# Kernel optimization log

Measured on AMD Instinct MI355X. Metric: run time of the kernel, lower is better.

Reference implementation:

```python
import jax, jax.numpy as jnp
import numpy as np

N, E, F, H = 50000, 800000, 128, 128
HEADS, HOUT, NUM_GRAPHS, NUM_CLASSES, L = 4, 32, 50, 2, 3
BN_EPS = 1e-5


def setup_inputs() -> dict:
    key = jax.random.key(0)
    it = iter(jax.random.split(key, 64))
    def nrm(shape, scale=0.1):
        return scale * jax.random.normal(next(it), shape, jnp.float32)
    npg = N // NUM_GRAPHS  # nodes per graph = 1000
    # edges constrained to stay within a single graph
    src = jax.random.randint(next(it), (E,), 0, npg, jnp.int32)
    dst = jax.random.randint(next(it), (E,), 0, npg, jnp.int32)
    goff = jax.random.randint(next(it), (E,), 0, NUM_GRAPHS, jnp.int32) * npg
    return dict(
        x=jax.random.normal(next(it), (N, F), jnp.float32),
        edge_index=jnp.stack([src + goff, dst + goff]),
        batch=jnp.arange(N, dtype=jnp.int32) // npg,
        W_gcn=nrm((F, H)), b_gcn=nrm((H,)),
        gin_W1=nrm((F, H)), gin_b1=nrm((H,)), gin_W2=nrm((H, H)), gin_b2=nrm((H,)),
        W_gat=nrm((F, HEADS * HOUT)), b_gat=nrm((HEADS * HOUT,)),
        a_src=nrm((HEADS, HOUT)), a_dst=nrm((HEADS, HOUT)),
        gat_proj_W=nrm((HEADS * HOUT, H)), gat_proj_b=nrm((H,)),
        gate_W1=nrm((3 * H, H)), gate_b1=nrm((H,)), gate_W2=nrm((H, 3)), gate_b2=nrm((3,)),
        bn0_g=jnp.ones((H,), jnp.float32) + nrm((H,)), bn0_b=nrm((H,)),
        conv_rel_W=nrm((L, H, H)), conv_rel_b=nrm((L, H)), conv_root_W=nrm((L, H, H)),
        bn_g=jnp.ones((L, H), jnp.float32) + nrm((L, H)), bn_b=nrm((L, H)),
        jump_W=nrm((L * H, H)), jump_b=nrm((H,)),
        att_W1=nrm((H, H)), att_b1=nrm((H,)), att_W2=nrm((H, 1)), att_b2=nrm((1,)),
        comb_W=nrm((4 * H, H)), comb_b=nrm((H,)),
        cls_W1=nrm((H, H // 2)), cls_b1=nrm((H // 2,)),
        cls_W2=nrm((H // 2, NUM_CLASSES)), cls_b2=nrm((NUM_CLASSES,)),
    )


def _forward(x, edge_index, batch, W_gcn, b_gcn, gin_W1, gin_b1, gin_W2, gin_b2,
             W_gat, b_gat, a_src, a_dst, gat_proj_W, gat_proj_b,
             gate_W1, gate_b1, gate_W2, gate_b2, bn0_g, bn0_b,
             conv_rel_W, conv_rel_b, conv_root_W, bn_g, bn_b, jump_W, jump_b,
             att_W1, att_b1, att_W2, att_b2, comb_W, comb_b,
             cls_W1, cls_b1, cls_W2, cls_b2):
    relu = jax.nn.relu
    seg_sum, seg_max = jax.ops.segment_sum, jax.ops.segment_max
    n = x.shape[0]
    src, dst = edge_index[0], edge_index[1]
    loop = jnp.arange(n, dtype=src.dtype)
    src_sl = jnp.concatenate([src, loop])  # self-loops (GCN/GAT add them)
    dst_sl = jnp.concatenate([dst, loop])

    def bn(h, g, b):  # eval-mode BatchNorm1d, running mean=0, var=1
        return h * (g / jnp.sqrt(1.0 + BN_EPS)) + b

    # --- GCN stem: sym-normalized A+I ---
    deg = seg_sum(jnp.ones_like(dst_sl, jnp.float32), dst_sl, num_segments=n)
    dinv = jax.lax.rsqrt(deg)  # deg >= 1 thanks to self-loops
    norm = dinv[src_sl] * dinv[dst_sl]
    h = x @ W_gcn
    x_gcn = relu(seg_sum(h[src_sl] * norm[:, None], dst_sl, num_segments=n) + b_gcn)

    # --- GIN stem: MLP((1+0)*x + sum_j x_j), no self-loops ---
    aggr = seg_sum(x[src], dst, num_segments=n)
    x_gin = relu(relu((x + aggr) @ gin_W1 + gin_b1) @ gin_W2 + gin_b2)

    # --- GAT stem: per-edge attention, segment softmax over dst ---
    xp = (x @ W_gat).reshape(n, HEADS, HOUT)
    al_s = (xp * a_src).sum(-1)  # [n, heads]
    al_d = (xp * a_dst).sum(-1)
    e = jax.nn.leaky_relu(al_s[src_sl] + al_d[dst_sl], 0.2)  # [E+n, heads]
    m = seg_max(e, dst_sl, num_segments=n)
    ex = jnp.exp(e - m[dst_sl])
    alpha = ex / seg_sum(ex, dst_sl, num_segments=n)[dst_sl]
    x_gat = seg_sum(xp[src_sl] * alpha[:, :, None], dst_sl, num_segments=n)
    x_gat = x_gat.reshape(n, HEADS * HOUT) + b_gat
    x_gat = relu(x_gat) @ gat_proj_W + gat_proj_b

    # --- gated fusion ---
    x_cat = jnp.concatenate([x_gcn, x_gin, x_gat], axis=-1)
    gates = jax.nn.softmax(relu(x_cat @ gate_W1 + gate_b1) @ gate_W2 + gate_b2, axis=-1)
    xx = gates[:, 0:1] * x_gcn + gates[:, 1:2] * x_gin + gates[:, 2:3] * x_gat
    xx = relu(bn(xx, bn0_g, bn0_b))  # dropout = no-op in eval

    # --- GraphConv stack with residuals (IdentityPooling since use_sag=False) ---
    reps = []
    for i in range(L):
        x_in = xx
        a = seg_sum(xx[src], dst, num_segments=n)  # aggr='add'
        h = a @ conv_rel_W[i] + conv_rel_b[i] + xx @ conv_root_W[i]
        xx = relu(bn(h, bn_g[i], bn_b[i])) + x_in
        reps.append(xx)

    xx = jnp.concatenate(reps, axis=-1) @ jump_W + jump_b  # JK cat

    # --- combo global pooling: mean / max / add / att ---
    cnt = seg_sum(jnp.ones((n,), jnp.float32), batch, num_segments=NUM_GRAPHS)
    x_add = seg_sum(xx, batch, num_segments=NUM_GRAPHS)
    x_mean = x_add / cnt[:, None]
    x_max = seg_max(xx, batch, num_segments=NUM_GRAPHS)
    a_log = (relu(xx @ att_W1 + att_b1) @ att_W2 + att_b2)[:, 0]  # [n]
    mg = seg_max(a_log, batch, num_segments=NUM_GRAPHS)
    exg = jnp.exp(a_log - mg[batch])
    att = exg / seg_sum(exg, batch, num_segments=NUM_GRAPHS)[batch]
    x_att = seg_sum(xx * att[:, None], batch, num_segments=NUM_GRAPHS)
    hg = jnp.concatenate([x_mean, x_max, x_add, x_att], axis=-1) @ comb_W + comb_b

    return relu(hg @ cls_W1 + cls_b1) @ cls_W2 + cls_b2  # [NUM_GRAPHS, NUM_CLASSES]


def reference(x, edge_index, batch, W_gcn, b_gcn, gin_W1, gin_b1, gin_W2, gin_b2,
              W_gat, b_gat, a_src, a_dst, gat_proj_W, gat_proj_b,
              gate_W1, gate_b1, gate_W2, gate_b2, bn0_g, bn0_b,
              conv_rel_W, conv_rel_b, conv_root_W, bn_g, bn_b, jump_W, jump_b,
              att_W1, att_b1, att_W2, att_b2, comb_W, comb_b,
              cls_W1, cls_b1, cls_W2, cls_b2):
    return _forward(x, edge_index, batch, W_gcn, b_gcn, gin_W1, gin_b1, gin_W2, gin_b2,
                    W_gat, b_gat, a_src, a_dst, gat_proj_W, gat_proj_b,
                    gate_W1, gate_b1, gate_W2, gate_b2, bn0_g, bn0_b,
                    conv_rel_W, conv_rel_b, conv_root_W, bn_g, bn_b, jump_W, jump_b,
                    att_W1, att_b1, att_W2, att_b2, comb_W, comb_b,
                    cls_W1, cls_b1, cls_W2, cls_b2)
```

## Files before the change

### kernel.cpp

```cpp
#include <hip/hip_runtime.h>

typedef float f32x4 __attribute__((ext_vector_type(4)));
typedef short s16x8 __attribute__((ext_vector_type(8)));

#define LDA 136

static __device__ __forceinline__ unsigned short f2bf(float f){
  union { float f; unsigned int u; } v; v.f = f;
  unsigned int u = v.u;
  return (unsigned short)((u + 0x7fffu + ((u >> 16) & 1u)) >> 16);
}
static __device__ __forceinline__ float2 bfp2f(unsigned int p){
  union { unsigned int u; float f; } a, b;
  a.u = (p & 0xffffu) << 16; b.u = p & 0xffff0000u;
  return make_float2(a.f, b.f);
}
static __device__ __forceinline__ unsigned int f2bfp(float x, float y){
  return (unsigned int)f2bf(x) | ((unsigned int)f2bf(y) << 16);
}
static __device__ __forceinline__ float bf2f(unsigned short h){
  union { unsigned int u; float f; } v; v.u = (unsigned int)h << 16; return v.f;
}

static __device__ __forceinline__ float lrelu02(float x){ return x > 0.f ? x : 0.2f * x; }

static __device__ __forceinline__ int xcd_swz(int bid, int nwg){
  int q = nwg >> 3, r = nwg & 7, x = bid & 7, i = bid >> 3;
  return (x < r ? x * (q + 1) : r * (q + 1) + (x - r) * q) + i;
}


__global__ void zero_u32(unsigned int* p, int n){
  int i = blockIdx.x * 256 + threadIdx.x;
  if (i < n) p[i] = 0u;
}

__global__ void gcount_kernel(const int* __restrict__ dst, unsigned int* __restrict__ gcnt,
                              int E, int npg, int ng){
  __shared__ unsigned int h[64];
  int tid = threadIdx.x;
  if (tid < 64) h[tid] = 0u;
  __syncthreads();
  for (int i = blockIdx.x * 256 + tid; i < E; i += gridDim.x * 256)
    atomicAdd(&h[dst[i] / npg], 1u);
  __syncthreads();
  if (tid < ng) atomicAdd(&gcnt[tid], h[tid]);
}

__global__ void gscan_kernel(const unsigned int* __restrict__ gcnt, unsigned int* __restrict__ goff, int ng){
  if (threadIdx.x == 0){
    unsigned int run = 0;
    for (int i = 0; i < ng; ++i){ goff[i] = run; run += gcnt[i]; }
    goff[ng] = run;
  }
}

__global__ void gbucket_kernel(const int* __restrict__ src, const int* __restrict__ dst,
                               const unsigned int* __restrict__ goff, unsigned int* __restrict__ gfill,
                               int2* __restrict__ ebuf, int E, int npg, int ng){
  __shared__ unsigned int h[64];
  __shared__ unsigned int base[64];
  __shared__ unsigned int fl[64];
  int tid = threadIdx.x;
  if (tid < 64){ h[tid] = 0u; fl[tid] = 0u; }
  __syncthreads();
  int per = (E + gridDim.x - 1) / gridDim.x;
  int i0 = blockIdx.x * per, i1 = min(E, i0 + per);
  for (int i = i0 + tid; i < i1; i += 256)
    atomicAdd(&h[dst[i] / npg], 1u);
  __syncthreads();
  if (tid < ng) base[tid] = goff[tid] + atomicAdd(&gfill[tid], h[tid]);
  __syncthreads();
  for (int i = i0 + tid; i < i1; i += 256){
    int d = dst[i];
    int g = d / npg;
    unsigned int p = base[g] + atomicAdd(&fl[g], 1u);
    ebuf[p] = make_int2(src[i], d);
  }
}

__global__ void csr_graph_kernel(const int2* __restrict__ ebuf, const unsigned int* __restrict__ goff,
                                 unsigned int* __restrict__ rp, int* __restrict__ colA,
                                 int* __restrict__ dstA, float* __restrict__ dinv,
                                 int npg, int N, int Etot){
  __shared__ unsigned int hist[1024];
  __shared__ unsigned int fill[1024];
  int g = blockIdx.x, tid = threadIdx.x;
  unsigned int e0 = goff[g], e1 = goff[g + 1];
  int nbase = g * npg;
  hist[tid] = 0u; fill[tid] = 0u;
  __syncthreads();
  for (unsigned int e = e0 + tid; e < e1; e += 1024)
    atomicAdd(&hist[ebuf[e].y - nbase], 1u);
  __syncthreads();
  unsigned int cnt = hist[tid];
  for (int off = 1; off < 1024; off <<= 1){
    unsigned int t = (tid >= off) ? hist[tid - off] : 0u;
    __syncthreads();
    hist[tid] += t;
    __syncthreads();
  }
  unsigned int basev = e0 + hist[tid] - cnt;
  __syncthreads();
  hist[tid] = basev;
  if (tid < npg){
    int node = nbase + tid;
    rp[node] = basev;
    dinv[node] = rsqrtf((float)cnt + 1.0f);
  }
  if (g == 0 && tid == 0) rp[N] = (unsigned int)Etot;
  __syncthreads();
  for (unsigned int e = e0 + tid; e < e1; e += 1024){
    int2 sd = ebuf[e];
    int ld = sd.y - nbase;
    unsigned int pos = hist[ld] + atomicAdd(&fill[ld], 1u);
    colA[pos] = sd.x;
    dstA[pos] = sd.y;
  }
}

__global__ void xcast_kernel(const float* __restrict__ x, unsigned short* __restrict__ xb, int n2){
  int i = blockIdx.x * 256 + threadIdx.x;
  if (i < n2){
    float2 v = ((const float2*)x)[i];
    ((unsigned int*)xb)[i] = f2bfp(v.x, v.y);
  }
}

__global__ void ew_kernel(const int* __restrict__ colA, const int* __restrict__ dstA,
                          const float* __restrict__ als, const float* __restrict__ ald,
                          unsigned int* __restrict__ wb, int E){
  int i = blockIdx.x * 256 + threadIdx.x;
  if (i >= E) return;
  int s = colA[i], d = dstA[i];
  float4 as = ((const float4*)als)[s];
  float4 ad = ((const float4*)ald)[d];
  float w0 = __expf(fminf(lrelu02(as.x + ad.x), 30.f));
  float w1 = __expf(fminf(lrelu02(as.y + ad.y), 30.f));
  float w2 = __expf(fminf(lrelu02(as.z + ad.z), 30.f));
  float w3 = __expf(fminf(lrelu02(as.w + ad.w), 30.f));
  wb[(size_t)i * 2 + 0] = f2bfp(w0, w1);
  wb[(size_t)i * 2 + 1] = f2bfp(w2, w3);
}


struct WSrc { const float* p[18]; };

__global__ void wtrans_kernel(WSrc s, unsigned short* __restrict__ dstAll){
  const float* src = s.p[blockIdx.x];
  unsigned short* dst = dstAll + (size_t)blockIdx.x * 16384;
  __shared__ float st[64][129];
  int tid = threadIdx.x;
  int kb = blockIdx.y * 64;
#pragma unroll
  for (int j = 0; j < 8; ++j){
    int e = tid + 256 * j;
    int r = e >> 5, c4 = (e & 31) * 4;
    float4 v = *(const float4*)(src + (size_t)(kb + r) * 128 + c4);
    st[r][c4] = v.x; st[r][c4+1] = v.y; st[r][c4+2] = v.z; st[r][c4+3] = v.w;
  }
  __syncthreads();
#pragma unroll
  for (int j = 0; j < 8; ++j){
    int e = tid + 256 * j;
    int c = e >> 4, k4 = (e & 15) * 4;
    ushort4 o;
    o.x = f2bf(st[k4+0][c]); o.y = f2bf(st[k4+1][c]);
    o.z = f2bf(st[k4+2][c]); o.w = f2bf(st[k4+3][c]);
    *(ushort4*)(dst + (size_t)c * 128 + kb + k4) = o;
  }
}


template<int EPI>
__launch_bounds__(256, 2)
__global__ void gemm_kernel(const unsigned short* __restrict__ A0, const unsigned short* __restrict__ A1,
                            const unsigned short* __restrict__ A2,
                            const unsigned short* __restrict__ W0, const unsigned short* __restrict__ W1,
                            const unsigned short* __restrict__ W2,
                            const float* __restrict__ bias, const float* __restrict__ bng, const float* __restrict__ bnb,
                            const unsigned short* __restrict__ resid, unsigned short* __restrict__ C, int nrows)
{
  __shared__ unsigned short As[64 * LDA];
  __shared__ unsigned short Wt[128 * LDA];
  const int tid = threadIdx.x;
  const int wave = tid >> 6, lane = tid & 63;
  const int row0 = blockIdx.x * 64;
  const unsigned short* Aps[3] = {A0, A1, A2};
  const unsigned short* Wps[3] = {W0, W1, W2};
  f32x4 acc[8];
#pragma unroll
  for (int i = 0; i < 8; ++i) acc[i] = (f32x4){0.f, 0.f, 0.f, 0.f};

  for (int p = 0; p < 3; ++p){
    const unsigned short* Ap = Aps[p];
    if (Ap == nullptr) break;
    const unsigned short* Wp = Wps[p];
    if (p) __syncthreads();
#pragma unroll
    for (int j = 0; j < 4; ++j){
      int e = tid + 256 * j;
      int r = e >> 4, k8 = (e & 15) * 8;
      int gr = row0 + r;
      s16x8 v = {0,0,0,0,0,0,0,0};
      if (gr < nrows) v = *(const s16x8*)(Ap + (size_t)gr * 128 + k8);
      *(s16x8*)(As + r * LDA + k8) = v;
    }
#pragma unroll
    for (int j = 0; j < 8; ++j){
      int e = tid + 256 * j;
      int colw = e >> 4, k8 = (e & 15) * 8;
      *(s16x8*)(Wt + colw * LDA + k8) = *(const s16x8*)(Wp + (size_t)colw * 128 + k8);
    }
    __syncthreads();
#pragma unroll
    for (int kc = 0; kc < 4; ++kc){
      int ko = kc * 32 + (lane >> 4) * 8;
      s16x8 av = *(const s16x8*)(As + (wave * 16 + (lane & 15)) * LDA + ko);
#pragma unroll
      for (int ct = 0; ct < 8; ++ct){
        s16x8 bv = *(const s16x8*)(Wt + (ct * 16 + (lane & 15)) * LDA + ko);
        acc[ct] = __builtin_amdgcn_mfma_f32_16x16x32_bf16(av, bv, acc[ct], 0, 0, 0);
      }
    }
  }
  const float RSQ = 0.99999500003749969f;
#pragma unroll
  for (int ct = 0; ct < 8; ++ct){
    int colg = ct * 16 + (lane & 15);
    float bv_ = (EPI >= 1) ? bias[colg] : 0.f;
    float sg = (EPI == 3) ? bng[colg] * RSQ : 0.f;
    float sb = (EPI == 3) ? bnb[colg] : 0.f;
#pragma unroll
    for (int r = 0; r < 4; ++r){
      int rowg = row0 + wave * 16 + (lane >> 4) * 4 + r;
      if (rowg < nrows){
        float v = acc[ct][r];
        if (EPI == 1) v += bv_;
        else if (EPI == 2) v = fmaxf(v + bv_, 0.f);
        else if (EPI == 3){
          v = (v + bv_) * sg + sb;
          v = fmaxf(v, 0.f) + bf2f(resid[(size_t)rowg * 128 + colg]);
        }
        C[(size_t)rowg * 128 + colg] = f2bf(v);
      }
    }
  }
}

__launch_bounds__(256, 2)
__global__ void gemm_dual_kernel(const unsigned short* __restrict__ A,
                                 const unsigned short* __restrict__ W0, const unsigned short* __restrict__ W1,
                                 const float* __restrict__ dscale,
                                 unsigned short* __restrict__ C0, unsigned short* __restrict__ C1, int nrows)
{
  __shared__ unsigned short As[64 * LDA];
  __shared__ unsigned short Wt[128 * LDA];
  const int tid = threadIdx.x;
  const int wave = tid >> 6, lane = tid & 63;
  const int row0 = blockIdx.x * 64;
  f32x4 acc0[8], acc1[8];
#pragma unroll
  for (int i = 0; i < 8; ++i){ acc0[i] = (f32x4){0.f,0.f,0.f,0.f}; acc1[i] = (f32x4){0.f,0.f,0.f,0.f}; }

#pragma unroll
  for (int j = 0; j < 4; ++j){
    int e = tid + 256 * j;
    int r = e >> 4, k8 = (e & 15) * 8;
    int gr = row0 + r;
    s16x8 v = {0,0,0,0,0,0,0,0};
    if (gr < nrows) v = *(const s16x8*)(A + (size_t)gr * 128 + k8);
    *(s16x8*)(As + r * LDA + k8) = v;
  }
#pragma unroll
  for (int j = 0; j < 8; ++j){
    int e = tid + 256 * j;
    int colw = e >> 4, k8 = (e & 15) * 8;
    *(s16x8*)(Wt + colw * LDA + k8) = *(const s16x8*)(W0 + (size_t)colw * 128 + k8);
  }
  __syncthreads();
  s16x8 av[4];
#pragma unroll
  for (int kc = 0; kc < 4; ++kc)
    av[kc] = *(const s16x8*)(As + (wave * 16 + (lane & 15)) * LDA + kc * 32 + (lane >> 4) * 8);
#pragma unroll
  for (int kc = 0; kc < 4; ++kc){
    int ko = kc * 32 + (lane >> 4) * 8;
#pragma unroll
    for (int ct = 0; ct < 8; ++ct){
      s16x8 bv = *(const s16x8*)(Wt + (ct * 16 + (lane & 15)) * LDA + ko);
      acc0[ct] = __builtin_amdgcn_mfma_f32_16x16x32_bf16(av[kc], bv, acc0[ct], 0, 0, 0);
    }
  }
  __syncthreads();
#pragma unroll
  for (int j = 0; j < 8; ++j){
    int e = tid + 256 * j;
    int colw = e >> 4, k8 = (e & 15) * 8;
    *(s16x8*)(Wt + colw * LDA + k8) = *(const s16x8*)(W1 + (size_t)colw * 128 + k8);
  }
  __syncthreads();
#pragma unroll
  for (int kc = 0; kc < 4; ++kc){
    int ko = kc * 32 + (lane >> 4) * 8;
#pragma unroll
    for (int ct = 0; ct < 8; ++ct){
      s16x8 bv = *(const s16x8*)(Wt + (ct * 16 + (lane & 15)) * LDA + ko);
      acc1[ct] = __builtin_amdgcn_mfma_f32_16x16x32_bf16(av[kc], bv, acc1[ct], 0, 0, 0);
    }
  }
#pragma unroll
  for (int ct = 0; ct < 8; ++ct){
    int colg = ct * 16 + (lane & 15);
#pragma unroll
    for (int r = 0; r < 4; ++r){
      int rowg = row0 + wave * 16 + (lane >> 4) * 4 + r;
      if (rowg < nrows){
        C0[(size_t)rowg * 128 + colg] = f2bf(acc0[ct][r] * dscale[rowg]);
        C1[(size_t)rowg * 128 + colg] = f2bf(acc1[ct][r]);
      }
    }
  }
}


__global__ void gin_agg_kernel(const unsigned short* __restrict__ x, const unsigned int* __restrict__ rp,
                               const int* __restrict__ col, unsigned short* __restrict__ xs, int n){
  int bid = xcd_swz(blockIdx.x, gridDim.x);
  int node = bid * 4 + (int)(threadIdx.x >> 6);
  if (node >= n) return;
  int lane = threadIdx.x & 63;
  const unsigned int* xin = (const unsigned int*)x;
  float2 acc = bfp2f(xin[(size_t)node * 64 + lane]);
  unsigned int rs = rp[node], re = rp[node + 1], e = rs;
  for (; e + 4 <= re; e += 4){
    int s0 = col[e], s1 = col[e+1], s2 = col[e+2], s3 = col[e+3];
    float2 v0 = bfp2f(xin[(size_t)s0 * 64 + lane]);
    float2 v1 = bfp2f(xin[(size_t)s1 * 64 + lane]);
    float2 v2 = bfp2f(xin[(size_t)s2 * 64 + lane]);
    float2 v3 = bfp2f(xin[(size_t)s3 * 64 + lane]);
    acc.x += v0.x + v1.x + v2.x + v3.x;
    acc.y += v0.y + v1.y + v2.y + v3.y;
  }
  for (; e < re; ++e){
    float2 v = bfp2f(xin[(size_t)col[e] * 64 + lane]);
    acc.x += v.x; acc.y += v.y;
  }
  ((unsigned int*)xs)[(size_t)node * 64 + lane] = f2bfp(acc.x, acc.y);
}

__global__ void gcn_agg_kernel(const unsigned short* __restrict__ hd, const float* __restrict__ dinv,
                               const unsigned int* __restrict__ rp, const int* __restrict__ col,
                               const float* __restrict__ b, unsigned short* __restrict__ out, int n){
  int bid = xcd_swz(blockIdx.x, gridDim.x);
  int node = bid * 4 + (int)(threadIdx.x >> 6);
  if (node >= n) return;
  int lane = threadIdx.x & 63;
  const unsigned int* hv = (const unsigned int*)hd;
  float di = dinv[node];
  float2 acc = bfp2f(hv[(size_t)node * 64 + lane]);
  unsigned int rs = rp[node], re = rp[node + 1], e = rs;
  for (; e + 4 <= re; e += 4){
    int s0 = col[e], s1 = col[e+1], s2 = col[e+2], s3 = col[e+3];
    float2 v0 = bfp2f(hv[(size_t)s0 * 64 + lane]);
    float2 v1 = bfp2f(hv[(size_t)s1 * 64 + lane]);
    float2 v2 = bfp2f(hv[(size_t)s2 * 64 + lane]);
    float2 v3 = bfp2f(hv[(size_t)s3 * 64 + lane]);
    acc.x += v0.x + v1.x + v2.x + v3.x;
    acc.y += v0.y + v1.y + v2.y + v3.y;
  }
  for (; e < re; ++e){
    float2 v = bfp2f(hv[(size_t)col[e] * 64 + lane]);
    acc.x += v.x; acc.y += v.y;
  }
  int f = lane * 2;
  float o0 = fmaxf(acc.x * di + b[f], 0.f);
  float o1 = fmaxf(acc.y * di + b[f + 1], 0.f);
  ((unsigned int*)out)[(size_t)node * 64 + lane] = f2bfp(o0, o1);
}

__global__ void sum_agg_kernel(const unsigned short* __restrict__ x, const unsigned int* __restrict__ rp,
                               const int* __restrict__ col, unsigned short* __restrict__ out, int n){
  int bid = xcd_swz(blockIdx.x, gridDim.x);
  int node = bid * 4 + (int)(threadIdx.x >> 6);
  if (node >= n) return;
  int lane = threadIdx.x & 63;
  const unsigned int* xin = (const unsigned int*)x;
  float2 acc = make_float2(0.f, 0.f);
  unsigned int rs = rp[node], re = rp[node + 1], e = rs;
  for (; e + 4 <= re; e += 4){
    int s0 = col[e], s1 = col[e+1], s2 = col[e+2], s3 = col[e+3];
    float2 v0 = bfp2f(xin[(size_t)s0 * 64 + lane]);
    float2 v1 = bfp2f(xin[(size_t)s1 * 64 + lane]);
    float2 v2 = bfp2f(xin[(size_t)s2 * 64 + lane]);
    float2 v3 = bfp2f(xin[(size_t)s3 * 64 + lane]);
    acc.x += v0.x + v1.x + v2.x + v3.x;
    acc.y += v0.y + v1.y + v2.y + v3.y;
  }
  for (; e < re; ++e){
    float2 v = bfp2f(xin[(size_t)col[e] * 64 + lane]);
    acc.x += v.x; acc.y += v.y;
  }
  ((unsigned int*)out)[(size_t)node * 64 + lane] = f2bfp(acc.x, acc.y);
}

__global__ void gat_agg_kernel(const unsigned short* __restrict__ xp, const float* __restrict__ als,
                               const float* __restrict__ ald, const unsigned int* __restrict__ wb,
                               const unsigned int* __restrict__ rp, const int* __restrict__ col,
                               const float* __restrict__ bgat, unsigned short* __restrict__ out, int n){
  int bid = xcd_swz(blockIdx.x, gridDim.x);
  int node = bid * 4 + (int)(threadIdx.x >> 6);
  if (node >= n) return;
  int lane = threadIdx.x & 63;
  int h = lane >> 4;
  int wword = h >> 1, wsh = (h & 1) * 16;
  const unsigned int* xv = (const unsigned int*)xp;
  float w = __expf(fminf(lrelu02(als[(size_t)node * 4 + h] + ald[(size_t)node * 4 + h]), 30.f));
  float2 sv = bfp2f(xv[(size_t)node * 64 + lane]);
  float2 acc = make_float2(sv.x * w, sv.y * w);
  float denom = w;
  unsigned int rs = rp[node], re = rp[node + 1], e = rs;
  for (; e + 4 <= re; e += 4){
    int s0 = col[e], s1 = col[e+1], s2 = col[e+2], s3 = col[e+3];
    float w0 = bf2f((unsigned short)(wb[(size_t)(e+0) * 2 + wword] >> wsh));
    float w1 = bf2f((unsigned short)(wb[(size_t)(e+1) * 2 + wword] >> wsh));
    float w2 = bf2f((unsigned short)(wb[(size_t)(e+2) * 2 + wword] >> wsh));
    float w3 = bf2f((unsigned short)(wb[(size_t)(e+3) * 2 + wword] >> wsh));
    float2 v0 = bfp2f(xv[(size_t)s0 * 64 + lane]);
    float2 v1 = bfp2f(xv[(size_t)s1 * 64 + lane]);
    float2 v2 = bfp2f(xv[(size_t)s2 * 64 + lane]);
    float2 v3 = bfp2f(xv[(size_t)s3 * 64 + lane]);
    acc.x += v0.x * w0 + v1.x * w1 + v2.x * w2 + v3.x * w3;
    acc.y += v0.y * w0 + v1.y * w1 + v2.y * w2 + v3.y * w3;
    denom += w0 + w1 + w2 + w3;
  }
  for (; e < re; ++e){
    float we = bf2f((unsigned short)(wb[(size_t)e * 2 + wword] >> wsh));
    float2 v = bfp2f(xv[(size_t)col[e] * 64 + lane]);
    acc.x += v.x * we; acc.y += v.y * we;
    denom += we;
  }
  float inv = 1.0f / denom;
  int f = lane * 2;
  float o0 = fmaxf(acc.x * inv + bgat[f], 0.f);
  float o1 = fmaxf(acc.y * inv + bgat[f + 1], 0.f);
  ((unsigned int*)out)[(size_t)node * 64 + lane] = f2bfp(o0, o1);
}


__global__ void alpair_kernel(const unsigned short* __restrict__ xp, const float* __restrict__ a_src,
                              const float* __restrict__ a_dst, float* __restrict__ als,
                              float* __restrict__ ald, int n){
  int node = blockIdx.x * 4 + (int)(threadIdx.x >> 6);
  if (node >= n) return;
  int lane = threadIdx.x & 63;
  int f = lane * 2;
  float2 v = bfp2f(((const unsigned int*)xp)[(size_t)node * 64 + lane]);
  float ps = v.x * a_src[f] + v.y * a_src[f + 1];
  float pd = v.x * a_dst[f] + v.y * a_dst[f + 1];
#pragma unroll
  for (int off = 1; off < 16; off <<= 1){
    ps += __shfl_xor(ps, off, 64);
    pd += __shfl_xor(pd, off, 64);
  }
  if ((lane & 15) == 0){
    int hh = lane >> 4;
    als[(size_t)node * 4 + hh] = ps;
    ald[(size_t)node * 4 + hh] = pd;
  }
}

__global__ void combine_kernel(const unsigned short* __restrict__ t, const float* __restrict__ W2,
                               const float* __restrict__ b2, const unsigned short* __restrict__ xg,
                               const unsigned short* __restrict__ xi, const unsigned short* __restrict__ xa,
                               const float* __restrict__ bn0g, const float* __restrict__ bn0b,
                               unsigned short* __restrict__ xx, int n){
  int node = blockIdx.x * 4 + (int)(threadIdx.x >> 6);
  if (node >= n) return;
  int lane = threadIdx.x & 63;
  int f = lane * 2;
  float2 tv = bfp2f(((const unsigned int*)t)[(size_t)node * 64 + lane]);
  float p0 = tv.x * W2[f * 3 + 0] + tv.y * W2[(f + 1) * 3 + 0];
  float p1 = tv.x * W2[f * 3 + 1] + tv.y * W2[(f + 1) * 3 + 1];
  float p2 = tv.x * W2[f * 3 + 2] + tv.y * W2[(f + 1) * 3 + 2];
#pragma unroll
  for (int off = 1; off < 64; off <<= 1){
    p0 += __shfl_xor(p0, off, 64);
    p1 += __shfl_xor(p1, off, 64);
    p2 += __shfl_xor(p2, off, 64);
  }
  p0 += b2[0]; p1 += b2[1]; p2 += b2[2];
  float mm = fmaxf(p0, fmaxf(p1, p2));
  float e0 = __expf(p0 - mm), e1 = __expf(p1 - mm), e2 = __expf(p2 - mm);
  float inv = 1.0f / (e0 + e1 + e2);
  e0 *= inv; e1 *= inv; e2 *= inv;
  float2 a = bfp2f(((const unsigned int*)xg)[(size_t)node * 64 + lane]);
  float2 b = bfp2f(((const unsigned int*)xi)[(size_t)node * 64 + lane]);
  float2 c = bfp2f(((const unsigned int*)xa)[(size_t)node * 64 + lane]);
  const float RSQ = 0.99999500003749969f;
  float o0 = fmaxf((e0 * a.x + e1 * b.x + e2 * c.x) * (bn0g[f] * RSQ) + bn0b[f], 0.f);
  float o1 = fmaxf((e0 * a.y + e1 * b.y + e2 * c.y) * (bn0g[f + 1] * RSQ) + bn0b[f + 1], 0.f);
  ((unsigned int*)xx)[(size_t)node * 64 + lane] = f2bfp(o0, o1);
}

__global__ void alog_kernel(const unsigned short* __restrict__ t, const float* __restrict__ w,
                            const float* __restrict__ b, float* __restrict__ alog, int n){
  int node = blockIdx.x * 4 + (int)(threadIdx.x >> 6);
  if (node >= n) return;
  int lane = threadIdx.x & 63;
  int f = lane * 2;
  float2 tv = bfp2f(((const unsigned int*)t)[(size_t)node * 64 + lane]);
  float p = tv.x * w[f] + tv.y * w[f + 1];
#pragma unroll
  for (int off = 1; off < 64; off <<= 1) p += __shfl_xor(p, off, 64);
  if (lane == 0) alog[node] = p + b[0];
}


__global__ void att_stats_kernel(const float* __restrict__ alog, float* __restrict__ gm,
                                 float* __restrict__ gz, int npg){
  __shared__ float red[256];
  int g = blockIdx.x, tid = threadIdx.x;
  size_t base = (size_t)g * npg;
  float m = -1e30f;
  for (int i = tid; i < npg; i += 256) m = fmaxf(m, alog[base + i]);
  red[tid] = m; __syncthreads();
  for (int off = 128; off > 0; off >>= 1){ if (tid < off) red[tid] = fmaxf(red[tid], red[tid + off]); __syncthreads(); }
  float gmax = red[0]; __syncthreads();
  float z = 0.f;
  for (int i = tid; i < npg; i += 256) z += __expf(alog[base + i] - gmax);
  red[tid] = z; __syncthreads();
  for (int off = 128; off > 0; off >>= 1){ if (tid < off) red[tid] += red[tid + off]; __syncthreads(); }
  if (tid == 0){ gm[g] = gmax; gz[g] = red[0]; }
}

__global__ void pool_partial_kernel(const unsigned short* __restrict__ xx, const float* __restrict__ alog,
                                    const float* __restrict__ gm, const float* __restrict__ gz,
                                    float* __restrict__ part, int npg, int nparts){
  __shared__ float wts[128];
  __shared__ float red[256];
  int g = blockIdx.x / nparts, p = blockIdx.x % nparts;
  int chunk = (npg + nparts - 1) / nparts;
  int n0 = p * chunk, n1 = min(npg, n0 + chunk);
  int tid = threadIdx.x;
  float gmax = gm[g], ginv = 1.0f / gz[g];
  size_t base = (size_t)g * npg;
  for (int i = n0 + tid; i < n1; i += 256) wts[i - n0] = __expf(alog[base + i] - gmax) * ginv;
  __syncthreads();
  int f = tid & 127, half = tid >> 7;
  float add = 0.f, mx = -1e30f, att = 0.f;
  for (int n2 = n0 + half; n2 < n1; n2 += 2){
    float v = bf2f(xx[(base + n2) * 128 + f]);
    add += v; mx = fmaxf(mx, v); att += v * wts[n2 - n0];
  }
  red[tid] = add; __syncthreads();
  float addf = add + ((half == 0) ? red[tid + 128] : 0.f);
  __syncthreads(); red[tid] = mx; __syncthreads();
  float mxf = (half == 0) ? fmaxf(mx, red[tid + 128]) : 0.f;
  __syncthreads(); red[tid] = att; __syncthreads();
  float attf = att + ((half == 0) ? red[tid + 128] : 0.f);
  if (half == 0){
    float* o = part + (size_t)(g * nparts + p) * 384;
    o[f] = addf; o[128 + f] = mxf; o[256 + f] = attf;
  }
}

__global__ void pool_final_kernel(const float* __restrict__ part, float* __restrict__ hg,
                                  int npg, int nparts){
  int g = blockIdx.x, f = threadIdx.x;
  float add = 0.f, mx = -1e30f, att = 0.f;
  for (int p = 0; p < nparts; ++p){
    const float* o = part + (size_t)(g * nparts + p) * 384;
    add += o[f]; mx = fmaxf(mx, o[128 + f]); att += o[256 + f];
  }
  float* o = hg + (size_t)g * 512;
  o[f] = add / (float)npg;
  o[128 + f] = mx;
  o[256 + f] = add;
  o[384 + f] = att;
}

__global__ void head_kernel(const float* __restrict__ hg, const float* __restrict__ combW,
                            const float* __restrict__ combB, const float* __restrict__ c1W,
                            const float* __restrict__ c1B, const float* __restrict__ c2W,
                            const float* __restrict__ c2B, float* __restrict__ out){
  __shared__ float cat[512];
  __shared__ float h1[128];
  __shared__ float h2[64];
  int g = blockIdx.x, tid = threadIdx.x;
#pragma unroll
  for (int j = 0; j < 4; ++j) cat[tid + 128 * j] = hg[(size_t)g * 512 + tid + 128 * j];
  __syncthreads();
  float a = combB[tid];
  for (int k = 0; k < 512; ++k) a += cat[k] * combW[(size_t)k * 128 + tid];
  h1[tid] = a; __syncthreads();
  if (tid < 64){
    float b = c1B[tid];
    for (int k = 0; k < 128; ++k) b += h1[k] * c1W[(size_t)k * 64 + tid];
    h2[tid] = fmaxf(b, 0.f);
  }
  __syncthreads();
  if (tid < 2){
    float o = c2B[tid];
    for (int k = 0; k < 64; ++k) o += h2[k] * c2W[(size_t)k * 2 + tid];
    out[(size_t)g * 2 + tid] = o;
  }
}


static void launch_gemm(int epi, dim3 grid, hipStream_t st,
                        const unsigned short* A0, const unsigned short* A1, const unsigned short* A2,
                        const unsigned short* W0, const unsigned short* W1, const unsigned short* W2,
                        const float* bias, const float* bng, const float* bnb,
                        const unsigned short* resid, unsigned short* C, int nrows){
  switch (epi){
    case 0: gemm_kernel<0><<<grid, 256, 0, st>>>(A0, A1, A2, W0, W1, W2, bias, bng, bnb, resid, C, nrows); break;
    case 1: gemm_kernel<1><<<grid, 256, 0, st>>>(A0, A1, A2, W0, W1, W2, bias, bng, bnb, resid, C, nrows); break;
    case 2: gemm_kernel<2><<<grid, 256, 0, st>>>(A0, A1, A2, W0, W1, W2, bias, bng, bnb, resid, C, nrows); break;
    default: gemm_kernel<3><<<grid, 256, 0, st>>>(A0, A1, A2, W0, W1, W2, bias, bng, bnb, resid, C, nrows); break;
  }
}

extern "C" void kernel_launch(void* const* d_in, const int* in_sizes, int n_in,
                              void* d_out, int out_size, void* d_ws, size_t ws_size,
                              hipStream_t stream){
  (void)n_in; (void)out_size; (void)ws_size;
  const int N = in_sizes[0] / 128;
  const int E = in_sizes[1] / 2;
  const int NG = 50;
  const int npg = N / NG;

  const float* x       = (const float*)d_in[0];
  const int*   ei      = (const int*)d_in[1];
  const int*   srcI    = ei;
  const int*   dstI    = ei + E;
  const float* W_gcn   = (const float*)d_in[3];
  const float* b_gcn   = (const float*)d_in[4];
  const float* gin_W1  = (const float*)d_in[5];
  const float* gin_b1  = (const float*)d_in[6];
  const float* gin_W2  = (const float*)d_in[7];
  const float* gin_b2  = (const float*)d_in[8];
  const float* W_gat   = (const float*)d_in[9];
  const float* b_gat   = (const float*)d_in[10];
  const float* a_src   = (const float*)d_in[11];
  const float* a_dst   = (const float*)d_in[12];
  const float* gproj_W = (const float*)d_in[13];
  const float* gproj_b = (const float*)d_in[14];
  const float* gate_W1 = (const float*)d_in[15];
  const float* gate_b1 = (const float*)d_in[16];
  const float* gate_W2 = (const float*)d_in[17];
  const float* gate_b2 = (const float*)d_in[18];
  const float* bn0_g   = (const float*)d_in[19];
  const float* bn0_b   = (const float*)d_in[20];
  const float* rel_W   = (const float*)d_in[21];
  const float* rel_b   = (const float*)d_in[22];
  const float* root_W  = (const float*)d_in[23];
  const float* bn_g    = (const float*)d_in[24];
  const float* bn_b    = (const float*)d_in[25];
  const float* jump_W  = (const float*)d_in[26];
  const float* jump_b  = (const float*)d_in[27];
  const float* att_W1  = (const float*)d_in[28];
  const float* att_b1  = (const float*)d_in[29];
  const float* att_W2  = (const float*)d_in[30];
  const float* att_b2  = (const float*)d_in[31];
  const float* comb_W  = (const float*)d_in[32];
  const float* comb_b  = (const float*)d_in[33];
  const float* cls_W1  = (const float*)d_in[34];
  const float* cls_b1  = (const float*)d_in[35];
  const float* cls_W2  = (const float*)d_in[36];
  const float* cls_b2  = (const float*)d_in[37];
  float* out = (float*)d_out;

  char* wp = (char*)d_ws;
  auto alloc = [&](size_t b) -> char* {
    char* p = wp; wp += (b + 511) & ~(size_t)511; return p;
  };
  unsigned int* rp   = (unsigned int*)alloc(((size_t)N + 1) * 4);
  int* colA          = (int*)alloc((size_t)E * 4);
  int* dstA          = (int*)alloc((size_t)E * 4);
  int2* ebuf         = (int2*)alloc((size_t)E * 8);
  unsigned int* wb   = (unsigned int*)alloc((size_t)E * 8);
  unsigned int* gcnt = (unsigned int*)alloc(192 * 4);
  unsigned int* gfill= gcnt + 64;
  unsigned int* goff = gcnt + 128;
  float* dinv        = (float*)alloc((size_t)N * 4);
  float* als         = (float*)alloc((size_t)N * 16);
  float* ald         = (float*)alloc((size_t)N * 16);
  float* alogv       = (float*)alloc((size_t)N * 4);
  unsigned short* WtAll = (unsigned short*)alloc((size_t)18 * 16384 * 2);
  float* hg          = (float*)alloc((size_t)NG * 512 * 4);
  float* gmv         = (float*)alloc((size_t)NG * 4);
  float* gzv         = (float*)alloc((size_t)NG * 4);
  int nparts = (npg + 99) / 100;
  float* part        = (float*)alloc((size_t)NG * nparts * 384 * 4);
  unsigned short* xbf = (unsigned short*)alloc((size_t)N * 128 * 2);
  unsigned short* S0 = (unsigned short*)alloc((size_t)N * 128 * 2);
  unsigned short* S1 = (unsigned short*)alloc((size_t)N * 128 * 2);
  unsigned short* S2 = (unsigned short*)alloc((size_t)N * 128 * 2);
  unsigned short* S3 = (unsigned short*)alloc((size_t)N * 128 * 2);
  unsigned short* S4 = (unsigned short*)alloc((size_t)N * 128 * 2);

  zero_u32<<<1, 256, 0, stream>>>(gcnt, 128);
  gcount_kernel<<<256, 256, 0, stream>>>(dstI, gcnt, E, npg, NG);
  gscan_kernel<<<1, 64, 0, stream>>>(gcnt, goff, NG);
  gbucket_kernel<<<256, 256, 0, stream>>>(srcI, dstI, goff, gfill, ebuf, E, npg, NG);
  csr_graph_kernel<<<NG, 1024, 0, stream>>>(ebuf, goff, rp, colA, dstA, dinv, npg, N, E);

  WSrc wsrc;
  wsrc.p[0] = W_gcn;  wsrc.p[1] = W_gat;  wsrc.p[2] = gin_W1; wsrc.p[3] = gin_W2;
  wsrc.p[4] = gproj_W;
  wsrc.p[5] = gate_W1;      wsrc.p[6] = gate_W1 + 16384; wsrc.p[7] = gate_W1 + 32768;
  wsrc.p[8] = rel_W;        wsrc.p[9] = rel_W + 16384;   wsrc.p[10] = rel_W + 32768;
  wsrc.p[11] = root_W;      wsrc.p[12] = root_W + 16384; wsrc.p[13] = root_W + 32768;
  wsrc.p[14] = jump_W;      wsrc.p[15] = jump_W + 16384; wsrc.p[16] = jump_W + 32768;
  wsrc.p[17] = att_W1;
  wtrans_kernel<<<dim3(18, 2), 256, 0, stream>>>(wsrc, WtAll);
  xcast_kernel<<<(N * 64 + 255) / 256, 256, 0, stream>>>(x, xbf, N * 64);

  dim3 gg((N + 63) / 64);
  int nb4 = (N + 3) / 4;
  #define WT(i) (WtAll + (size_t)(i) * 16384)
  const unsigned short* Z = nullptr;
  const unsigned short* BZ = nullptr;

  gemm_dual_kernel<<<gg, 256, 0, stream>>>(xbf, WT(0), WT(1), dinv, S0, S1, N);
  alpair_kernel<<<nb4, 256, 0, stream>>>(S1, a_src, a_dst, als, ald, N);
  ew_kernel<<<(E + 255) / 256, 256, 0, stream>>>(colA, dstA, als, ald, wb, E);
  gin_agg_kernel<<<nb4, 256, 0, stream>>>(xbf, rp, colA, S2, N);
  launch_gemm(2, gg, stream, S2, BZ, BZ, WT(2), Z, Z, gin_b1, nullptr, nullptr, BZ, S3, N);
  launch_gemm(2, gg, stream, S3, BZ, BZ, WT(3), Z, Z, gin_b2, nullptr, nullptr, BZ, S2, N);
  gcn_agg_kernel<<<nb4, 256, 0, stream>>>(S0, dinv, rp, colA, b_gcn, S3, N);
  gat_agg_kernel<<<nb4, 256, 0, stream>>>(S1, als, ald, wb, rp, colA, b_gat, S0, N);
  launch_gemm(1, gg, stream, S0, BZ, BZ, WT(4), Z, Z, gproj_b, nullptr, nullptr, BZ, S1, N);

  launch_gemm(2, gg, stream, S3, S2, S1, WT(5), WT(6), WT(7), gate_b1, nullptr, nullptr, BZ, S4, N);
  combine_kernel<<<nb4, 256, 0, stream>>>(S4, gate_W2, gate_b2, S3, S2, S1, bn0_g, bn0_b, S0, N);

  sum_agg_kernel<<<nb4, 256, 0, stream>>>(S0, rp, colA, S1, N);
  launch_gemm(3, gg, stream, S1, S0, BZ, WT(8), WT(11), Z, rel_b, bn_g, bn_b, S0, S2, N);
  sum_agg_kernel<<<nb4, 256, 0, stream>>>(S2, rp, colA, S1, N);
  launch_gemm(3, gg, stream, S1, S2, BZ, WT(9), WT(12), Z, rel_b + 128, bn_g + 128, bn_b + 128, S2, S3, N);
  sum_agg_kernel<<<nb4, 256, 0, stream>>>(S3, rp, colA, S1, N);
  launch_gemm(3, gg, stream, S1, S3, BZ, WT(10), WT(13), Z, rel_b + 256, bn_g + 256, bn_b + 256, S3, S4, N);

  launch_gemm(1, gg, stream, S2, S3, S4, WT(14), WT(15), WT(16), jump_b, nullptr, nullptr, BZ, S0, N);
  launch_gemm(2, gg, stream, S0, BZ, BZ, WT(17), Z, Z, att_b1, nullptr, nullptr, BZ, S1, N);
  alog_kernel<<<nb4, 256, 0, stream>>>(S1, att_W2, att_b2, alogv, N);

  att_stats_kernel<<<NG, 256, 0, stream>>>(alogv, gmv, gzv, npg);
  pool_partial_kernel<<<NG * nparts, 256, 0, stream>>>(S0, alogv, gmv, gzv, part, npg, nparts);
  pool_final_kernel<<<NG, 128, 0, stream>>>(part, hg, npg, nparts);
  head_kernel<<<NG, 128, 0, stream>>>(hg, comb_W, comb_b, cls_W1, cls_b1, cls_W2, cls_b2, out);
}
```

Before: 653.9 us.

## Fuse back-to-back GEMMs and row-reduction epilogues into single kernels

Merges the two GIN MLP GEMMs into one kernel that keeps the intermediate tile in shared memory. It also folds the gate softmax/combine step into the gate GEMM epilogue, and fuses the jump-knowledge GEMM with the attention MLP and its logit reduction. The goal is to drop several launches and the global-memory round trips for the intermediate N×128 activations. In exchange, the fused kernels do more per-block work and more shuffle reductions, and the buffer assignments are reshuffled.

```diff
diff --git a/kernel.cpp b/kernel.cpp
--- a/kernel.cpp
+++ b/kernel.cpp
@@ -171,6 +171,37 @@
   }
 }
 
+
+#define STAGE_A(Ap)                                            \
+  _Pragma("unroll")                                            \
+  for (int j = 0; j < 4; ++j){                                 \
+    int e = tid + 256 * j;                                     \
+    int r = e >> 4, k8 = (e & 15) * 8;                         \
+    int gr = row0 + r;                                         \
+    s16x8 v = {0,0,0,0,0,0,0,0};                               \
+    if (gr < nrows) v = *(const s16x8*)((Ap) + (size_t)gr * 128 + k8); \
+    *(s16x8*)(As + r * LDA + k8) = v;                          \
+  }
+
+#define STAGE_W(Wp)                                            \
+  _Pragma("unroll")                                            \
+  for (int j = 0; j < 8; ++j){                                 \
+    int e = tid + 256 * j;                                     \
+    int colw = e >> 4, k8 = (e & 15) * 8;                      \
+    *(s16x8*)(Wt + colw * LDA + k8) = *(const s16x8*)((Wp) + (size_t)colw * 128 + k8); \
+  }
+
+#define MFMA_LOOP(accv)                                        \
+  _Pragma("unroll")                                            \
+  for (int kc = 0; kc < 4; ++kc){                              \
+    int ko = kc * 32 + (lane >> 4) * 8;                        \
+    s16x8 av = *(const s16x8*)(As + (wave * 16 + (lane & 15)) * LDA + ko); \
+    _Pragma("unroll")                                          \
+    for (int ct = 0; ct < 8; ++ct){                            \
+      s16x8 bv = *(const s16x8*)(Wt + (ct * 16 + (lane & 15)) * LDA + ko); \
+      accv[ct] = __builtin_amdgcn_mfma_f32_16x16x32_bf16(av, bv, accv[ct], 0, 0, 0); \
+    }                                                          \
+  }
 
 template<int EPI>
 __launch_bounds__(256, 2)
@@ -197,38 +228,16 @@
     if (Ap == nullptr) break;
     const unsigned short* Wp = Wps[p];
     if (p) __syncthreads();
-#pragma unroll
-    for (int j = 0; j < 4; ++j){
-      int e = tid + 256 * j;
-      int r = e >> 4, k8 = (e & 15) * 8;
-      int gr = row0 + r;
-      s16x8 v = {0,0,0,0,0,0,0,0};
-      if (gr < nrows) v = *(const s16x8*)(Ap + (size_t)gr * 128 + k8);
-      *(s16x8*)(As + r * LDA + k8) = v;
-    }
-#pragma unroll
-    for (int j = 0; j < 8; ++j){
-      int e = tid + 256 * j;
-      int colw = e >> 4, k8 = (e & 15) * 8;
-      *(s16x8*)(Wt + colw * LDA + k8) = *(const s16x8*)(Wp + (size_t)colw * 128 + k8);
-    }
+    STAGE_A(Ap)
+    STAGE_W(Wp)
     __syncthreads();
-#pragma unroll
-    for (int kc = 0; kc < 4; ++kc){
-      int ko = kc * 32 + (lane >> 4) * 8;
-      s16x8 av = *(const s16x8*)(As + (wave * 16 + (lane & 15)) * LDA + ko);
-#pragma unroll
-      for (int ct = 0; ct < 8; ++ct){
-        s16x8 bv = *(const s16x8*)(Wt + (ct * 16 + (lane & 15)) * LDA + ko);
-        acc[ct] = __builtin_amdgcn_mfma_f32_16x16x32_bf16(av, bv, acc[ct], 0, 0, 0);
-      }
-    }
+    MFMA_LOOP(acc)
   }
   const float RSQ = 0.99999500003749969f;
 #pragma unroll
   for (int ct = 0; ct < 8; ++ct){
     int colg = ct * 16 + (lane & 15);
-    float bv_ = (EPI >= 1) ? bias[colg] : 0.f;
+    float bv_ = bias[colg];
     float sg = (EPI == 3) ? bng[colg] * RSQ : 0.f;
     float sb = (EPI == 3) ? bnb[colg] : 0.f;
 #pragma unroll
@@ -237,8 +246,7 @@
       if (rowg < nrows){
         float v = acc[ct][r];
         if (EPI == 1) v += bv_;
-        else if (EPI == 2) v = fmaxf(v + bv_, 0.f);
-        else if (EPI == 3){
+        else {
           v = (v + bv_) * sg + sb;
           v = fmaxf(v, 0.f) + bf2f(resid[(size_t)rowg * 128 + colg]);
         }
@@ -263,21 +271,8 @@
 #pragma unroll
   for (int i = 0; i < 8; ++i){ acc0[i] = (f32x4){0.f,0.f,0.f,0.f}; acc1[i] = (f32x4){0.f,0.f,0.f,0.f}; }
 
-#pragma unroll
-  for (int j = 0; j < 4; ++j){
-    int e = tid + 256 * j;
-    int r = e >> 4, k8 = (e & 15) * 8;
-    int gr = row0 + r;
-    s16x8 v = {0,0,0,0,0,0,0,0};
-    if (gr < nrows) v = *(const s16x8*)(A + (size_t)gr * 128 + k8);
-    *(s16x8*)(As + r * LDA + k8) = v;
-  }
-#pragma unroll
-  for (int j = 0; j < 8; ++j){
-    int e = tid + 256 * j;
-    int colw = e >> 4, k8 = (e & 15) * 8;
-    *(s16x8*)(Wt + colw * LDA + k8) = *(const s16x8*)(W0 + (size_t)colw * 128 + k8);
-  }
+  STAGE_A(A)
+  STAGE_W(W0)
   __syncthreads();
   s16x8 av[4];
 #pragma unroll
@@ -293,12 +288,7 @@
     }
   }
   __syncthreads();
-#pragma unroll
-  for (int j = 0; j < 8; ++j){
-    int e = tid + 256 * j;
-    int colw = e >> 4, k8 = (e & 15) * 8;
-    *(s16x8*)(Wt + colw * LDA + k8) = *(const s16x8*)(W1 + (size_t)colw * 128 + k8);
-  }
+  STAGE_W(W1)
   __syncthreads();
 #pragma unroll
   for (int kc = 0; kc < 4; ++kc){
@@ -319,6 +309,199 @@
         C0[(size_t)rowg * 128 + colg] = f2bf(acc0[ct][r] * dscale[rowg]);
         C1[(size_t)rowg * 128 + colg] = f2bf(acc1[ct][r]);
       }
+    }
+  }
+}
+
+__launch_bounds__(256, 2)
+__global__ void gemm_gin_kernel(const unsigned short* __restrict__ A,
+                                const unsigned short* __restrict__ W1, const unsigned short* __restrict__ W2,
+                                const float* __restrict__ b1, const float* __restrict__ b2,
+                                unsigned short* __restrict__ C, int nrows)
+{
+  __shared__ unsigned short As[64 * LDA];
+  __shared__ unsigned short Wt[128 * LDA];
+  const int tid = threadIdx.x;
+  const int wave = tid >> 6, lane = tid & 63;
+  const int row0 = blockIdx.x * 64;
+  f32x4 acc[8];
+#pragma unroll
+  for (int i = 0; i < 8; ++i) acc[i] = (f32x4){0.f,0.f,0.f,0.f};
+  STAGE_A(A)
+  STAGE_W(W1)
+  __syncthreads();
+  MFMA_LOOP(acc)
+  __syncthreads();
+#pragma unroll
+  for (int ct = 0; ct < 8; ++ct){
+    int colg = ct * 16 + (lane & 15);
+    float bb = b1[colg];
+#pragma unroll
+    for (int r = 0; r < 4; ++r){
+      int rl = wave * 16 + (lane >> 4) * 4 + r;
+      As[rl * LDA + colg] = f2bf(fmaxf(acc[ct][r] + bb, 0.f));
+    }
+  }
+  STAGE_W(W2)
+#pragma unroll
+  for (int i = 0; i < 8; ++i) acc[i] = (f32x4){0.f,0.f,0.f,0.f};
+  __syncthreads();
+  MFMA_LOOP(acc)
+#pragma unroll
+  for (int ct = 0; ct < 8; ++ct){
+    int colg = ct * 16 + (lane & 15);
+    float bb = b2[colg];
+#pragma unroll
+    for (int r = 0; r < 4; ++r){
+      int rowg = row0 + wave * 16 + (lane >> 4) * 4 + r;
+      if (rowg < nrows)
+        C[(size_t)rowg * 128 + colg] = f2bf(fmaxf(acc[ct][r] + bb, 0.f));
+    }
+  }
+}
+
+__launch_bounds__(256, 2)
+__global__ void gemm_gate_kernel(const unsigned short* __restrict__ A0, const unsigned short* __restrict__ A1,
+                                 const unsigned short* __restrict__ A2,
+                                 const unsigned short* __restrict__ W0, const unsigned short* __restrict__ W1,
+                                 const unsigned short* __restrict__ W2w,
+                                 const float* __restrict__ b1, const float* __restrict__ gW2,
+                                 const float* __restrict__ gb2,
+                                 const float* __restrict__ bn0g, const float* __restrict__ bn0b,
+                                 unsigned short* __restrict__ XX, int nrows)
+{
+  __shared__ unsigned short As[64 * LDA];
+  __shared__ unsigned short Wt[128 * LDA];
+  const int tid = threadIdx.x;
+  const int wave = tid >> 6, lane = tid & 63;
+  const int row0 = blockIdx.x * 64;
+  const unsigned short* Aps[3] = {A0, A1, A2};
+  const unsigned short* Wps[3] = {W0, W1, W2w};
+  f32x4 acc[8];
+#pragma unroll
+  for (int i = 0; i < 8; ++i) acc[i] = (f32x4){0.f,0.f,0.f,0.f};
+  for (int p = 0; p < 3; ++p){
+    if (p) __syncthreads();
+    STAGE_A(Aps[p])
+    STAGE_W(Wps[p])
+    __syncthreads();
+    MFMA_LOOP(acc)
+  }
+  float p0[4] = {0,0,0,0}, p1[4] = {0,0,0,0}, p2[4] = {0,0,0,0};
+#pragma unroll
+  for (int ct = 0; ct < 8; ++ct){
+    int colg = ct * 16 + (lane & 15);
+    float bb = b1[colg];
+    float w0 = gW2[colg * 3 + 0], w1 = gW2[colg * 3 + 1], w2 = gW2[colg * 3 + 2];
+#pragma unroll
+    for (int r = 0; r < 4; ++r){
+      float t = fmaxf(acc[ct][r] + bb, 0.f);
+      p0[r] += t * w0; p1[r] += t * w1; p2[r] += t * w2;
+    }
+  }
+#pragma unroll
+  for (int off = 1; off < 16; off <<= 1){
+#pragma unroll
+    for (int r = 0; r < 4; ++r){
+      p0[r] += __shfl_xor(p0[r], off, 64);
+      p1[r] += __shfl_xor(p1[r], off, 64);
+      p2[r] += __shfl_xor(p2[r], off, 64);
+    }
+  }
+  float e0[4], e1[4], e2[4];
+#pragma unroll
+  for (int r = 0; r < 4; ++r){
+    float q0 = p0[r] + gb2[0], q1 = p1[r] + gb2[1], q2 = p2[r] + gb2[2];
+    float mm = fmaxf(q0, fmaxf(q1, q2));
+    float x0 = __expf(q0 - mm), x1 = __expf(q1 - mm), x2 = __expf(q2 - mm);
+    float inv = 1.0f / (x0 + x1 + x2);
+    e0[r] = x0 * inv; e1[r] = x1 * inv; e2[r] = x2 * inv;
+  }
+  const float RSQ = 0.99999500003749969f;
+#pragma unroll
+  for (int ct = 0; ct < 8; ++ct){
+    int colg = ct * 16 + (lane & 15);
+    float sg = bn0g[colg] * RSQ, sb = bn0b[colg];
+#pragma unroll
+    for (int r = 0; r < 4; ++r){
+      int rowg = row0 + wave * 16 + (lane >> 4) * 4 + r;
+      if (rowg < nrows){
+        float a = bf2f(A0[(size_t)rowg * 128 + colg]);
+        float b = bf2f(A1[(size_t)rowg * 128 + colg]);
+        float c = bf2f(A2[(size_t)rowg * 128 + colg]);
+        float o = fmaxf((e0[r] * a + e1[r] * b + e2[r] * c) * sg + sb, 0.f);
+        XX[(size_t)rowg * 128 + colg] = f2bf(o);
+      }
+    }
+  }
+}
+
+__launch_bounds__(256, 2)
+__global__ void gemm_jump_att_kernel(const unsigned short* __restrict__ A0, const unsigned short* __restrict__ A1,
+                                     const unsigned short* __restrict__ A2,
+                                     const unsigned short* __restrict__ W0, const unsigned short* __restrict__ W1,
+                                     const unsigned short* __restrict__ W2w,
+                                     const float* __restrict__ jb,
+                                     const unsigned short* __restrict__ Wa, const float* __restrict__ ab1,
+                                     const float* __restrict__ aw2, const float* __restrict__ ab2,
+                                     unsigned short* __restrict__ XX2, float* __restrict__ alog, int nrows)
+{
+  __shared__ unsigned short As[64 * LDA];
+  __shared__ unsigned short Wt[128 * LDA];
+  const int tid = threadIdx.x;
+  const int wave = tid >> 6, lane = tid & 63;
+  const int row0 = blockIdx.x * 64;
+  const unsigned short* Aps[3] = {A0, A1, A2};
+  const unsigned short* Wps[3] = {W0, W1, W2w};
+  f32x4 acc[8];
+#pragma unroll
+  for (int i = 0; i < 8; ++i) acc[i] = (f32x4){0.f,0.f,0.f,0.f};
+  for (int p = 0; p < 3; ++p){
+    if (p) __syncthreads();
+    STAGE_A(Aps[p])
+    STAGE_W(Wps[p])
+    __syncthreads();
+    MFMA_LOOP(acc)
+  }
+  __syncthreads();
+#pragma unroll
+  for (int ct = 0; ct < 8; ++ct){
+    int colg = ct * 16 + (lane & 15);
+    float bb = jb[colg];
+#pragma unroll
+    for (int r = 0; r < 4; ++r){
+      int rl = wave * 16 + (lane >> 4) * 4 + r;
+      unsigned short h = f2bf(acc[ct][r] + bb);
+      As[rl * LDA + colg] = h;
+      int rowg = row0 + rl;
+      if (rowg < nrows) XX2[(size_t)rowg * 128 + colg] = h;
+    }
+  }
+  STAGE_W(Wa)
+#pragma unroll
+  for (int i = 0; i < 8; ++i) acc[i] = (f32x4){0.f,0.f,0.f,0.f};
+  __syncthreads();
+  MFMA_LOOP(acc)
+  float pl[4] = {0,0,0,0};
+#pragma unroll
+  for (int ct = 0; ct < 8; ++ct){
+    int colg = ct * 16 + (lane & 15);
+    float bb = ab1[colg];
+    float w = aw2[colg];
+#pragma unroll
+    for (int r = 0; r < 4; ++r)
+      pl[r] += fmaxf(acc[ct][r] + bb, 0.f) * w;
+  }
+#pragma unroll
+  for (int off = 1; off < 16; off <<= 1){
+#pragma unroll
+    for (int r = 0; r < 4; ++r) pl[r] += __shfl_xor(pl[r], off, 64);
+  }
+  if ((lane & 15) == 0){
+#pragma unroll
+    for (int r = 0; r < 4; ++r){
+      int rowg = row0 + wave * 16 + (lane >> 4) * 4 + r;
+      if (rowg < nrows) alog[rowg] = pl[r] + ab2[0];
     }
   }
 }
@@ -470,52 +653,6 @@
   }
 }
 
-__global__ void combine_kernel(const unsigned short* __restrict__ t, const float* __restrict__ W2,
-                               const float* __restrict__ b2, const unsigned short* __restrict__ xg,
-                               const unsigned short* __restrict__ xi, const unsigned short* __restrict__ xa,
-                               const float* __restrict__ bn0g, const float* __restrict__ bn0b,
-                               unsigned short* __restrict__ xx, int n){
-  int node = blockIdx.x * 4 + (int)(threadIdx.x >> 6);
-  if (node >= n) return;
-  int lane = threadIdx.x & 63;
-  int f = lane * 2;
-  float2 tv = bfp2f(((const unsigned int*)t)[(size_t)node * 64 + lane]);
-  float p0 = tv.x * W2[f * 3 + 0] + tv.y * W2[(f + 1) * 3 + 0];
-  float p1 = tv.x * W2[f * 3 + 1] + tv.y * W2[(f + 1) * 3 + 1];
-  float p2 = tv.x * W2[f * 3 + 2] + tv.y * W2[(f + 1) * 3 + 2];
-#pragma unroll
-  for (int off = 1; off < 64; off <<= 1){
-    p0 += __shfl_xor(p0, off, 64);
-    p1 += __shfl_xor(p1, off, 64);
-    p2 += __shfl_xor(p2, off, 64);
-  }
-  p0 += b2[0]; p1 += b2[1]; p2 += b2[2];
-  float mm = fmaxf(p0, fmaxf(p1, p2));
-  float e0 = __expf(p0 - mm), e1 = __expf(p1 - mm), e2 = __expf(p2 - mm);
-  float inv = 1.0f / (e0 + e1 + e2);
-  e0 *= inv; e1 *= inv; e2 *= inv;
-  float2 a = bfp2f(((const unsigned int*)xg)[(size_t)node * 64 + lane]);
-  float2 b = bfp2f(((const unsigned int*)xi)[(size_t)node * 64 + lane]);
-  float2 c = bfp2f(((const unsigned int*)xa)[(size_t)node * 64 + lane]);
-  const float RSQ = 0.99999500003749969f;
-  float o0 = fmaxf((e0 * a.x + e1 * b.x + e2 * c.x) * (bn0g[f] * RSQ) + bn0b[f], 0.f);
-  float o1 = fmaxf((e0 * a.y + e1 * b.y + e2 * c.y) * (bn0g[f + 1] * RSQ) + bn0b[f + 1], 0.f);
-  ((unsigned int*)xx)[(size_t)node * 64 + lane] = f2bfp(o0, o1);
-}
-
-__global__ void alog_kernel(const unsigned short* __restrict__ t, const float* __restrict__ w,
-                            const float* __restrict__ b, float* __restrict__ alog, int n){
-  int node = blockIdx.x * 4 + (int)(threadIdx.x >> 6);
-  if (node >= n) return;
-  int lane = threadIdx.x & 63;
-  int f = lane * 2;
-  float2 tv = bfp2f(((const unsigned int*)t)[(size_t)node * 64 + lane]);
-  float p = tv.x * w[f] + tv.y * w[f + 1];
-#pragma unroll
-  for (int off = 1; off < 64; off <<= 1) p += __shfl_xor(p, off, 64);
-  if (lane == 0) alog[node] = p + b[0];
-}
-
 
 __global__ void att_stats_kernel(const float* __restrict__ alog, float* __restrict__ gm,
                                  float* __restrict__ gz, int npg){
@@ -607,19 +744,6 @@
   }
 }
 
-
-static void launch_gemm(int epi, dim3 grid, hipStream_t st,
-                        const unsigned short* A0, const unsigned short* A1, const unsigned short* A2,
-                        const unsigned short* W0, const unsigned short* W1, const unsigned short* W2,
-                        const float* bias, const float* bng, const float* bnb,
-                        const unsigned short* resid, unsigned short* C, int nrows){
-  switch (epi){
-    case 0: gemm_kernel<0><<<grid, 256, 0, st>>>(A0, A1, A2, W0, W1, W2, bias, bng, bnb, resid, C, nrows); break;
-    case 1: gemm_kernel<1><<<grid, 256, 0, st>>>(A0, A1, A2, W0, W1, W2, bias, bng, bnb, resid, C, nrows); break;
-    case 2: gemm_kernel<2><<<grid, 256, 0, st>>>(A0, A1, A2, W0, W1, W2, bias, bng, bnb, resid, C, nrows); break;
-    default: gemm_kernel<3><<<grid, 256, 0, st>>>(A0, A1, A2, W0, W1, W2, bias, bng, bnb, resid, C, nrows); break;
-  }
-}
 
 extern "C" void kernel_launch(void* const* d_in, const int* in_sizes, int n_in,
                               void* d_out, int out_size, void* d_ws, size_t ws_size,
@@ -727,25 +851,23 @@
   alpair_kernel<<<nb4, 256, 0, stream>>>(S1, a_src, a_dst, als, ald, N);
   ew_kernel<<<(E + 255) / 256, 256, 0, stream>>>(colA, dstA, als, ald, wb, E);
   gin_agg_kernel<<<nb4, 256, 0, stream>>>(xbf, rp, colA, S2, N);
-  launch_gemm(2, gg, stream, S2, BZ, BZ, WT(2), Z, Z, gin_b1, nullptr, nullptr, BZ, S3, N);
-  launch_gemm(2, gg, stream, S3, BZ, BZ, WT(3), Z, Z, gin_b2, nullptr, nullptr, BZ, S2, N);
-  gcn_agg_kernel<<<nb4, 256, 0, stream>>>(S0, dinv, rp, colA, b_gcn, S3, N);
+  gemm_gin_kernel<<<gg, 256, 0, stream>>>(S2, WT(2), WT(3), gin_b1, gin_b2, S3, N);
+  gcn_agg_kernel<<<nb4, 256, 0, stream>>>(S0, dinv, rp, colA, b_gcn, S4, N);
   gat_agg_kernel<<<nb4, 256, 0, stream>>>(S1, als, ald, wb, rp, colA, b_gat, S0, N);
-  launch_gemm(1, gg, stream, S0, BZ, BZ, WT(4), Z, Z, gproj_b, nullptr, nullptr, BZ, S1, N);
-
-  launch_gemm(2, gg, stream, S3, S2, S1, WT(5), WT(6), WT(7), gate_b1, nullptr, nullptr, BZ, S4, N);
-  combine_kernel<<<nb4, 256, 0, stream>>>(S4, gate_W2, gate_b2, S3, S2, S1, bn0_g, bn0_b, S0, N);
-
-  sum_agg_kernel<<<nb4, 256, 0, stream>>>(S0, rp, colA, S1, N);
-  launch_gemm(3, gg, stream, S1, S0, BZ, WT(8), WT(11), Z, rel_b, bn_g, bn_b, S0, S2, N);
-  sum_agg_kernel<<<nb4, 256, 0, stream>>>(S2, rp, colA, S1, N);
-  launch_gemm(3, gg, stream, S1, S2, BZ, WT(9), WT(12), Z, rel_b + 128, bn_g + 128, bn_b + 128, S2, S3, N);
-  sum_agg_kernel<<<nb4, 256, 0, stream>>>(S3, rp, colA, S1, N);
-  launch_gemm(3, gg, stream, S1, S3, BZ, WT(10), WT(13), Z, rel_b + 256, bn_g + 256, bn_b + 256, S3, S4, N);
-
-  launch_gemm(1, gg, stream, S2, S3, S4, WT(14), WT(15), WT(16), jump_b, nullptr, nullptr, BZ, S0, N);
-  launch_gemm(2, gg, stream, S0, BZ, BZ, WT(17), Z, Z, att_b1, nullptr, nullptr, BZ, S1, N);
-  alog_kernel<<<nb4, 256, 0, stream>>>(S1, att_W2, att_b2, alogv, N);
+  gemm_kernel<1><<<gg, 256, 0, stream>>>(S0, BZ, BZ, WT(4), Z, Z, gproj_b, nullptr, nullptr, BZ, S1, N);
+
+  gemm_gate_kernel<<<gg, 256, 0, stream>>>(S4, S3, S1, WT(5), WT(6), WT(7),
+                                           gate_b1, gate_W2, gate_b2, bn0_g, bn0_b, S2, N);
+
+  sum_agg_kernel<<<nb4, 256, 0, stream>>>(S2, rp, colA, S0, N);
+  gemm_kernel<3><<<gg, 256, 0, stream>>>(S0, S2, BZ, WT(8), WT(11), Z, rel_b, bn_g, bn_b, S2, S1, N);
+  sum_agg_kernel<<<nb4, 256, 0, stream>>>(S1, rp, colA, S0, N);
+  gemm_kernel<3><<<gg, 256, 0, stream>>>(S0, S1, BZ, WT(9), WT(12), Z, rel_b + 128, bn_g + 128, bn_b + 128, S1, S4, N);
+  sum_agg_kernel<<<nb4, 256, 0, stream>>>(S4, rp, colA, S0, N);
+  gemm_kernel<3><<<gg, 256, 0, stream>>>(S0, S4, BZ, WT(10), WT(13), Z, rel_b + 256, bn_g + 256, bn_b + 256, S4, S2, N);
+
+  gemm_jump_att_kernel<<<gg, 256, 0, stream>>>(S1, S4, S2, WT(14), WT(15), WT(16), jump_b,
+                                               WT(17), att_b1, att_W2, att_b2, S0, alogv, N);
 
   att_stats_kernel<<<NG, 256, 0, stream>>>(alogv, gmv, gzv, npg);
   pool_partial_kernel<<<NG * nparts, 256, 0, stream>>>(S0, alogv, gmv, gzv, part, npg, nparts);
```

After: 625.6 us. 4.3% less time.
